# Kernel tuning notes

Measured on AMD Instinct MI355X. Metric: run time of the kernel, lower is better.

The kernel has to match this reference:

```python
import jax, jax.numpy as jnp
import numpy as np

H = 16          # bit depth; n = 2**H
K = 4           # f*H // division_fact = 2*16//8
TP = 8          # number of coordinate copies
N = 1 << H
T1 = 128        # query block
T2 = 512        # key block
D = 256         # euclidean embedding dim
C = 2 * K * H + 1  # connection candidates = 129


def _distance(c1, c2, norm):
    # sign/exponent 'critical graph' distance:
    # sg = sign(c1)*sign(c2); s = frexp_exponent(|c1|^|c2| + 1)/H
    sg = ((2 * (c1 >= 0).astype(jnp.int32) - 1) *
          (2 * (c2 >= 0).astype(jnp.int32) - 1)).astype(jnp.float32)
    xr = jnp.abs(c1) ^ jnp.abs(c2)
    _, e = jnp.frexp((xr + 1).astype(jnp.float32))
    return sg * (1.0 - e.astype(jnp.float32) / H) * norm


def setup_inputs() -> dict:
    key = jax.random.key(0)
    k1, k2, k3, k4, k5, k6 = jax.random.split(key, 6)
    emb_T1 = jax.random.normal(k1, (T1, D), jnp.float32)
    emb_T2 = jax.random.normal(k2, (T2, D), jnp.float32)
    # locations are signed integers in [1-n, n) as in __init__
    sta_loc = jax.random.randint(k3, (T1, TP), 1 - N, N, jnp.int32)
    pos_loc = jax.random.randint(k4, (T2, TP), 1 - N, N, jnp.int32)
    # neighbor valid_mask: choosing_mask = rand > 0.2
    mask = jax.random.bernoulli(k5, 0.8, (T1, T2))
    # raw random numbers for generate_random_masks (low-bit masks applied inside reference)
    random_masks = jax.random.randint(k6, (T1, H, K, TP), 0, N, jnp.int32)
    return {"emb_T1": emb_T1, "emb_T2": emb_T2, "sta_loc": sta_loc,
            "pos_loc": pos_loc, "mask": mask, "random_masks": random_masks}


def reference(emb_T1, emb_T2, sta_loc, pos_loc, mask, random_masks):
    # ---- connection(): bit-flip XOR candidate generation ----
    flip = (jnp.int32(1) << jnp.arange(H, dtype=jnp.int32))          # (H,)
    flipped = sta_loc[:, None, :] ^ flip[None, :, None]              # (T1, H, TP)
    low = random_masks & (flip - 1)[None, :, None, None]             # keep low i bits
    res = (flipped[:, :, None, :] ^ low).reshape(T1, H * K, TP)      # (T1, H*K, TP)
    cnc_loc = jnp.concatenate([res, sta_loc[:, None, :], -res], axis=1)  # (T1, C, TP)

    # ---- normalized_matmul -> target similarity val_v; val_n = ones ----
    e1 = emb_T1 / jnp.linalg.norm(emb_T1, axis=-1, keepdims=True)
    e2 = emb_T2 / jnp.linalg.norm(emb_T2, axis=-1, keepdims=True)
    val_v = e1 @ e2.T                                                # (T1, T2)

    # ---- distances (val_n == 1) ----
    dis_sta = _distance(sta_loc[:, None, :], pos_loc[None, :, :], 1.0)       # (T1,T2,TP)
    dsum = dis_sta.sum(-1)                                                   # (T1,T2)
    dis_cnc = _distance(cnc_loc[:, None, :, :], pos_loc[None, :, None, :], 1.0)  # (T1,T2,C,TP)
    ct_val = (dsum[:, :, None, None] - dis_sta[:, :, None, :] + dis_cnc) / TP    # (T1,T2,C,TP)

    # ---- masked MSE loss, summed over the T2 (neighbor) dim ----
    diff = ct_val - val_v[:, :, None, None]
    loss = (diff * diff * mask[:, :, None, None].astype(jnp.float32)).sum(axis=1)  # (T1,C,TP)
    return loss
```

## Files before the change

kernel.cpp:

```cpp
#include <hip/hip_runtime.h>
#include <stdint.h>

#define T1c 128
#define T2c 512
#define TPc 8
#define Cc  129
#define Dc  256
#define QT  128
#define MBS 132

__device__ __forceinline__ int pack_loc(int v) {
    int a = v < 0 ? -v : v;
    return a | (v < 0 ? (int)0x80000000 : 0);
}

__device__ __forceinline__ void dist_core(unsigned v1, unsigned v2, float& dd, float& val) {
    unsigned xv = v1 ^ v2;
    val = fmaf((float)__clz((int)((xv & 0x7FFFFFFFu) + 1u)), 0.0625f, -1.0f);
    dd  = __uint_as_float(__float_as_uint(val) ^ (xv & 0x80000000u));
}

__device__ __forceinline__ float wave_sum(float v) {
    #pragma unroll
    for (int off = 32; off; off >>= 1) v += __shfl_xor(v, off, 64);
    return v;
}

__global__ __launch_bounds__(256, 2) void k_fused(
    const float* __restrict__ e1, const float* __restrict__ e2,
    const int* __restrict__ sta, const int* __restrict__ pos,
    const void* __restrict__ mask, const int* __restrict__ rm,
    float* __restrict__ out) {
    int b  = blockIdx.x;
    int t1 = b >> 2;
    int q  = b & 3;
    int base = q * QT;
    int tid  = threadIdx.x;
    int lane = tid & 63;

    __shared__ float se1[Dc];
    __shared__ float sdot[256], sss[256];
    __shared__ float smbs[TPc][MBS];
    __shared__ int   spp[TPc][MBS];
    __shared__ float smf[QT];
    __shared__ float sred[2][9];
    __shared__ float sA[9];
    __shared__ float sB1[128][4], sQ1[128][4];
    __shared__ float sinv1;
    __shared__ int   sflag;

    if (tid == 0) sflag = 0;
    __syncthreads();
    if (((const unsigned char*)mask)[1 + 4 * tid] != 0) atomicOr(&sflag, 1);
    if (tid < 64) {
        float4 a = ((const float4*)(e1 + (size_t)t1 * Dc))[tid];
        ((float4*)se1)[tid] = a;
        float s = wave_sum(a.x * a.x + a.y * a.y + a.z * a.z + a.w * a.w);
        if (tid == 0) sinv1 = rsqrtf(s);
    }
    __syncthreads();

    {
        int t2 = base + (tid >> 1), h = tid & 1;
        const float4* xrow = (const float4*)(e2 + (size_t)t2 * Dc) + h * 32;
        const float4* arow = (const float4*)se1 + h * 32;
        float dx = 0.f, dy = 0.f, dz = 0.f, dw = 0.f;
        float sx = 0.f, sy = 0.f, sz = 0.f, sw = 0.f;
        #pragma unroll 8
        for (int d = 0; d < 32; ++d) {
            float4 x = xrow[d];
            float4 a = arow[d];
            dx = fmaf(a.x, x.x, dx); dy = fmaf(a.y, x.y, dy);
            dz = fmaf(a.z, x.z, dz); dw = fmaf(a.w, x.w, dw);
            sx = fmaf(x.x, x.x, sx); sy = fmaf(x.y, x.y, sy);
            sz = fmaf(x.z, x.z, sz); sw = fmaf(x.w, x.w, sw);
        }
        sdot[tid] = (dx + dy) + (dz + dw);
        sss[tid]  = (sx + sy) + (sz + sw);
    }
    __syncthreads();

    if (tid < QT) {
        int t2 = base + tid;
        float dot = sdot[2 * tid] + sdot[2 * tid + 1];
        float ss  = sss[2 * tid]  + sss[2 * tid + 1];
        float vv  = dot * sinv1 * rsqrtf(ss);
        int idx = t1 * T2c + t2;
        float m;
        if (sflag) m = (((const unsigned char*)mask)[idx] != 0) ? 1.0f : 0.0f;
        else       m = (((const int*)mask)[idx] != 0) ? 1.0f : 0.0f;
        smf[tid] = m;

        int4 p0 = ((const int4*)(pos + (size_t)t2 * TPc))[0];
        int4 p1 = ((const int4*)(pos + (size_t)t2 * TPc))[1];
        int pk[8] = {pack_loc(p0.x), pack_loc(p0.y), pack_loc(p0.z), pack_loc(p0.w),
                     pack_loc(p1.x), pack_loc(p1.y), pack_loc(p1.z), pack_loc(p1.w)};
        int4 s0 = ((const int4*)(sta + (size_t)t1 * TPc))[0];
        int4 s1 = ((const int4*)(sta + (size_t)t1 * TPc))[1];
        int sk[8] = {pack_loc(s0.x), pack_loc(s0.y), pack_loc(s0.z), pack_loc(s0.w),
                     pack_loc(s1.x), pack_loc(s1.y), pack_loc(s1.z), pack_loc(s1.w)};
        float d[8];
        float dsum = 0.f;
        #pragma unroll
        for (int p = 0; p < 8; ++p) {
            float dd, val;
            dist_core((unsigned)sk[p], (unsigned)pk[p], dd, val);
            d[p] = dd;
            dsum += dd;
        }
        float acc[9];
        #pragma unroll
        for (int p = 0; p < 8; ++p) {
            float mb = m * ((dsum - d[p]) * 0.125f - vv);
            smbs[p][tid] = __uint_as_float(__float_as_uint(mb) ^ ((unsigned)pk[p] & 0x80000000u));
            spp[p][tid]  = pk[p] & 0x7FFFFFFF;
            acc[p] = mb * mb;
        }
        float c6 = dsum * 0.125f - vv;
        acc[8] = m * c6 * c6;
        #pragma unroll
        for (int j = 0; j < 9; ++j) acc[j] = wave_sum(acc[j]);
        if (lane == 0) {
            #pragma unroll
            for (int j = 0; j < 9; ++j) sred[tid >> 6][j] = acc[j];
        }
    }
    __syncthreads();
    if (tid < 9) sA[tid] = sred[0][tid] + sred[1][tid];
    __syncthreads();

    int p  = tid & 7;
    int c0 = (tid >> 3) & 15;
    int u  = tid >> 7;
    int stav = sta[t1 * TPc + p];
    int resv[4], v1m[4];
    #pragma unroll
    for (int k = 0; k < 4; ++k) {
        int c = c0 + 16 * k;
        int i = c >> 2, kk = c & 3;
        int low = rm[(((t1 * 16 + i) * 4 + kk) * TPc) + p] & ((1 << i) - 1);
        int rv  = (stav ^ (1 << i)) ^ low;
        resv[k] = rv;
        v1m[k]  = rv < 0 ? -rv : rv;
    }

    const int4*   pp4 = (const int4*)&spp[p][u * 64];
    const float4* mb4 = (const float4*)&smbs[p][u * 64];
    const float4* mf4 = (const float4*)&smf[u * 64];

    float B[4] = {0.f, 0.f, 0.f, 0.f};
    float Q[4] = {0.f, 0.f, 0.f, 0.f};
    #pragma unroll 4
    for (int j = 0; j < 16; ++j) {
        int4   pv = pp4[j];
        float4 mb = mb4[j];
        float4 mm = mf4[j];
        #define EV(CMP) { \
            _Pragma("unroll") \
            for (int k = 0; k < 4; ++k) { \
                unsigned xr = (unsigned)v1m[k] ^ (unsigned)pv.CMP; \
                float val = fmaf((float)__clz((int)(xr + 1u)), 0.0625f, -1.0f); \
                B[k] = fmaf(mb.CMP, val, B[k]); \
                float t = mm.CMP * val; \
                Q[k] = fmaf(t, t, Q[k]); \
            } }
        EV(x) EV(y) EV(z) EV(w)
        #undef EV
    }

    if (u == 1) {
        int s = tid - 128;
        #pragma unroll
        for (int k = 0; k < 4; ++k) { sB1[s][k] = B[k]; sQ1[s][k] = Q[k]; }
    }
    __syncthreads();
    if (u == 0) {
        float A = sA[p];
        float* o = out + (size_t)t1 * Cc * TPc;
        #pragma unroll
        for (int k = 0; k < 4; ++k) {
            int c = c0 + 16 * k;
            float Bt = B[k] + sB1[tid][k];
            float Qt = Q[k] + sQ1[tid][k];
            float Bs = (resv[k] < 0) ? -Bt : Bt;
            float core = fmaf(Qt, 1.0f / 64.0f, A);
            float l0 = fmaf(Bs,  0.25f, core);
            float l1 = (resv[k] == 0) ? l0 : fmaf(Bs, -0.25f, core);
            atomicAdd(&o[c * TPc + p], l0);
            atomicAdd(&o[(65 + c) * TPc + p], l1);
        }
        if (tid < 8) atomicAdd(&o[64 * TPc + tid], sA[8]);
    }
}

extern "C" void kernel_launch(void* const* d_in, const int* in_sizes, int n_in,
                              void* d_out, int out_size, void* d_ws, size_t ws_size,
                              hipStream_t stream) {
    const float* emb1 = (const float*)d_in[0];
    const float* emb2 = (const float*)d_in[1];
    const int*   sta  = (const int*)d_in[2];
    const int*   pos  = (const int*)d_in[3];
    const void*  mask = d_in[4];
    const int*   rm   = (const int*)d_in[5];

    hipMemsetAsync(d_out, 0, (size_t)T1c * Cc * TPc * sizeof(float), stream);
    hipLaunchKernelGGL(k_fused, dim3(512), dim3(256), 0, stream,
                       emb1, emb2, sta, pos, mask, rm, (float*)d_out);
}
```

Measured before the change: 81.85 us.

## Split key dimension into 8 slices per query and expand loss algebraically

```diff
diff --git a/kernel.cpp b/kernel.cpp
--- a/kernel.cpp
+++ b/kernel.cpp
@@ -6,8 +6,8 @@
 #define TPc 8
 #define Cc  129
 #define Dc  256
-#define QT  128
-#define MBS 132
+#define ST  64
+#define MBS 68
 
 __device__ __forceinline__ int pack_loc(int v) {
     int a = v < 0 ? -v : v;
@@ -26,27 +26,23 @@
     return v;
 }
 
-__global__ __launch_bounds__(256, 2) void k_fused(
+__global__ __launch_bounds__(256, 4) void k_fused(
     const float* __restrict__ e1, const float* __restrict__ e2,
     const int* __restrict__ sta, const int* __restrict__ pos,
     const void* __restrict__ mask, const int* __restrict__ rm,
     float* __restrict__ out) {
     int b  = blockIdx.x;
-    int t1 = b >> 2;
-    int q  = b & 3;
-    int base = q * QT;
+    int t1 = b >> 3;
+    int s  = b & 7;
+    int base = s * ST;
     int tid  = threadIdx.x;
-    int lane = tid & 63;
 
     __shared__ float se1[Dc];
     __shared__ float sdot[256], sss[256];
     __shared__ float smbs[TPc][MBS];
     __shared__ int   spp[TPc][MBS];
-    __shared__ float smf[QT];
-    __shared__ float sred[2][9];
-    __shared__ float sA[9];
-    __shared__ float sB1[128][4], sQ1[128][4];
-    __shared__ float sinv1;
+    __shared__ float sA[TPc], sSb[TPc];
+    __shared__ float sSm, sC64, sinv1;
     __shared__ int   sflag;
 
     if (tid == 0) sflag = 0;
@@ -55,19 +51,19 @@
     if (tid < 64) {
         float4 a = ((const float4*)(e1 + (size_t)t1 * Dc))[tid];
         ((float4*)se1)[tid] = a;
-        float s = wave_sum(a.x * a.x + a.y * a.y + a.z * a.z + a.w * a.w);
-        if (tid == 0) sinv1 = rsqrtf(s);
+        float ssum = wave_sum(a.x * a.x + a.y * a.y + a.z * a.z + a.w * a.w);
+        if (tid == 0) sinv1 = rsqrtf(ssum);
     }
     __syncthreads();
 
     {
-        int t2 = base + (tid >> 1), h = tid & 1;
-        const float4* xrow = (const float4*)(e2 + (size_t)t2 * Dc) + h * 32;
-        const float4* arow = (const float4*)se1 + h * 32;
+        int t2 = base + (tid >> 2), h = tid & 3;
+        const float4* xrow = (const float4*)(e2 + (size_t)t2 * Dc) + h * 16;
+        const float4* arow = (const float4*)se1 + h * 16;
         float dx = 0.f, dy = 0.f, dz = 0.f, dw = 0.f;
         float sx = 0.f, sy = 0.f, sz = 0.f, sw = 0.f;
-        #pragma unroll 8
-        for (int d = 0; d < 32; ++d) {
+        #pragma unroll
+        for (int d = 0; d < 16; ++d) {
             float4 x = xrow[d];
             float4 a = arow[d];
             dx = fmaf(a.x, x.x, dx); dy = fmaf(a.y, x.y, dy);
@@ -80,16 +76,15 @@
     }
     __syncthreads();
 
-    if (tid < QT) {
+    if (tid < ST) {
         int t2 = base + tid;
-        float dot = sdot[2 * tid] + sdot[2 * tid + 1];
-        float ss  = sss[2 * tid]  + sss[2 * tid + 1];
+        float dot = (sdot[4 * tid] + sdot[4 * tid + 1]) + (sdot[4 * tid + 2] + sdot[4 * tid + 3]);
+        float ss  = (sss[4 * tid]  + sss[4 * tid + 1])  + (sss[4 * tid + 2]  + sss[4 * tid + 3]);
         float vv  = dot * sinv1 * rsqrtf(ss);
         int idx = t1 * T2c + t2;
         float m;
         if (sflag) m = (((const unsigned char*)mask)[idx] != 0) ? 1.0f : 0.0f;
         else       m = (((const int*)mask)[idx] != 0) ? 1.0f : 0.0f;
-        smf[tid] = m;
 
         int4 p0 = ((const int4*)(pos + (size_t)t2 * TPc))[0];
         int4 p1 = ((const int4*)(pos + (size_t)t2 * TPc))[1];
@@ -108,89 +103,87 @@
             d[p] = dd;
             dsum += dd;
         }
-        float acc[9];
+        float accA[8], accSb[8];
         #pragma unroll
         for (int p = 0; p < 8; ++p) {
-            float mb = m * ((dsum - d[p]) * 0.125f - vv);
-            smbs[p][tid] = __uint_as_float(__float_as_uint(mb) ^ ((unsigned)pk[p] & 0x80000000u));
-            spp[p][tid]  = pk[p] & 0x7FFFFFFF;
-            acc[p] = mb * mb;
+            float mb  = m * ((dsum - d[p]) * 0.125f - vv);
+            float mbs = __uint_as_float(__float_as_uint(mb) ^ ((unsigned)pk[p] & 0x80000000u));
+            smbs[p][tid] = mbs;
+            spp[p][tid]  = (m != 0.0f) ? (pk[p] & 0x7FFFFFFF) : (int)0xFFFC0000;
+            accA[p]  = mb * mb;
+            accSb[p] = mbs;
         }
         float c6 = dsum * 0.125f - vv;
-        acc[8] = m * c6 * c6;
-        #pragma unroll
-        for (int j = 0; j < 9; ++j) acc[j] = wave_sum(acc[j]);
-        if (lane == 0) {
+        float cA = m * c6 * c6;
+        #pragma unroll
+        for (int p = 0; p < 8; ++p) {
+            accA[p]  = wave_sum(accA[p]);
+            accSb[p] = wave_sum(accSb[p]);
+        }
+        float sm = wave_sum(m);
+        cA = wave_sum(cA);
+        if (tid == 0) {
             #pragma unroll
-            for (int j = 0; j < 9; ++j) sred[tid >> 6][j] = acc[j];
-        }
-    }
-    __syncthreads();
-    if (tid < 9) sA[tid] = sred[0][tid] + sred[1][tid];
+            for (int p = 0; p < 8; ++p) { sA[p] = accA[p]; sSb[p] = accSb[p]; }
+            sSm = sm;
+            sC64 = cA;
+        }
+    }
     __syncthreads();
 
     int p  = tid & 7;
-    int c0 = (tid >> 3) & 15;
-    int u  = tid >> 7;
+    int c0 = tid >> 3;
     int stav = sta[t1 * TPc + p];
-    int resv[4], v1m[4];
+    int resv[2];
+    unsigned v1m[2];
     #pragma unroll
-    for (int k = 0; k < 4; ++k) {
-        int c = c0 + 16 * k;
+    for (int k = 0; k < 2; ++k) {
+        int c = c0 + 32 * k;
         int i = c >> 2, kk = c & 3;
         int low = rm[(((t1 * 16 + i) * 4 + kk) * TPc) + p] & ((1 << i) - 1);
         int rv  = (stav ^ (1 << i)) ^ low;
         resv[k] = rv;
-        v1m[k]  = rv < 0 ? -rv : rv;
-    }
-
-    const int4*   pp4 = (const int4*)&spp[p][u * 64];
-    const float4* mb4 = (const float4*)&smbs[p][u * 64];
-    const float4* mf4 = (const float4*)&smf[u * 64];
-
-    float B[4] = {0.f, 0.f, 0.f, 0.f};
-    float Q[4] = {0.f, 0.f, 0.f, 0.f};
+        v1m[k]  = (unsigned)(rv < 0 ? -rv : rv);
+    }
+
+    const int4*   pp4 = (const int4*)&spp[p][0];
+    const float4* mb4 = (const float4*)&smbs[p][0];
+
+    float B0 = 0.f, B1 = 0.f, Qa0 = 0.f, Qa1 = 0.f, Qb0 = 0.f, Qb1 = 0.f;
     #pragma unroll 4
     for (int j = 0; j < 16; ++j) {
         int4   pv = pp4[j];
         float4 mb = mb4[j];
-        float4 mm = mf4[j];
         #define EV(CMP) { \
-            _Pragma("unroll") \
-            for (int k = 0; k < 4; ++k) { \
-                unsigned xr = (unsigned)v1m[k] ^ (unsigned)pv.CMP; \
-                float val = fmaf((float)__clz((int)(xr + 1u)), 0.0625f, -1.0f); \
-                B[k] = fmaf(mb.CMP, val, B[k]); \
-                float t = mm.CMP * val; \
-                Q[k] = fmaf(t, t, Q[k]); \
-            } }
+            unsigned x0 = v1m[0] ^ (unsigned)pv.CMP; \
+            unsigned x1 = v1m[1] ^ (unsigned)pv.CMP; \
+            float f0 = (float)__clz((int)(x0 + 1u)); \
+            float f1 = (float)__clz((int)(x1 + 1u)); \
+            B0 = fmaf(mb.CMP, f0, B0); B1 = fmaf(mb.CMP, f1, B1); \
+            Qa0 += f0; Qa1 += f1; \
+            Qb0 = fmaf(f0, f0, Qb0); Qb1 = fmaf(f1, f1, Qb1); }
         EV(x) EV(y) EV(z) EV(w)
         #undef EV
     }
 
-    if (u == 1) {
-        int s = tid - 128;
-        #pragma unroll
-        for (int k = 0; k < 4; ++k) { sB1[s][k] = B[k]; sQ1[s][k] = Q[k]; }
-    }
-    __syncthreads();
-    if (u == 0) {
-        float A = sA[p];
-        float* o = out + (size_t)t1 * Cc * TPc;
-        #pragma unroll
-        for (int k = 0; k < 4; ++k) {
-            int c = c0 + 16 * k;
-            float Bt = B[k] + sB1[tid][k];
-            float Qt = Q[k] + sQ1[tid][k];
-            float Bs = (resv[k] < 0) ? -Bt : Bt;
-            float core = fmaf(Qt, 1.0f / 64.0f, A);
-            float l0 = fmaf(Bs,  0.25f, core);
-            float l1 = (resv[k] == 0) ? l0 : fmaf(Bs, -0.25f, core);
-            atomicAdd(&o[c * TPc + p], l0);
-            atomicAdd(&o[(65 + c) * TPc + p], l1);
-        }
-        if (tid < 8) atomicAdd(&o[64 * TPc + tid], sA[8]);
-    }
+    float A = sA[p], Sb = sSb[p], Sm = sSm;
+    float* o = out + (size_t)t1 * Cc * TPc;
+    #pragma unroll
+    for (int k = 0; k < 2; ++k) {
+        int c = c0 + 32 * k;
+        float Bk = (k == 0) ? B0 : B1;
+        float Qak = (k == 0) ? Qa0 : Qa1;
+        float Qbk = (k == 0) ? Qb0 : Qb1;
+        float Bv = fmaf(Bk, 0.0625f, -Sb);
+        float Bs = (resv[k] < 0) ? -Bv : Bv;
+        float Qv = fmaf(Qbk, 1.0f / 256.0f, fmaf(Qak, -0.125f, Sm));
+        float core = fmaf(Qv, 1.0f / 64.0f, A);
+        float l0 = fmaf(Bs,  0.25f, core);
+        float l1 = (resv[k] == 0) ? l0 : fmaf(Bs, -0.25f, core);
+        atomicAdd(&o[c * TPc + p], l0);
+        atomicAdd(&o[(65 + c) * TPc + p], l1);
+    }
+    if (tid < 8) atomicAdd(&o[64 * TPc + tid], sC64);
 }
 
 extern "C" void kernel_launch(void* const* d_in, const int* in_sizes, int n_in,
@@ -204,6 +197,6 @@
     const int*   rm   = (const int*)d_in[5];
 
     hipMemsetAsync(d_out, 0, (size_t)T1c * Cc * TPc * sizeof(float), stream);
-    hipLaunchKernelGGL(k_fused, dim3(512), dim3(256), 0, stream,
+    hipLaunchKernelGGL(k_fused, dim3(1024), dim3(256), 0, stream,
                        emb1, emb2, sta, pos, mask, rm, (float*)d_out);
 }
```

Result: no change. 80.66 us (-1.4%).
